# Performance work log

Hardware: AMD Instinct MI355X
Metric: run time of the kernel (lower is better)

Reference implementation:

```python
import jax, jax.numpy as jnp
import numpy as np

B, L, E, H, W = 2, 4096, 512, 8, 128
D = E // H

def _clin(x, Wr, Wi, br, bi):
    # ComplexLinear on real input: out = x@(Wr + i*Wi)^T + (br + i*bi)
    return x @ Wr.T + br, x @ Wi.T + bi

def setup_inputs() -> dict:
    key = jax.random.key(0)
    ks = jax.random.split(key, 20)
    s = 0.02
    d = {
        'query': jax.random.normal(ks[0], (B, L, E), jnp.float32),
        'key':   jax.random.normal(ks[1], (B, L, E), jnp.float32),
        'value': jax.random.normal(ks[2], (B, L, E), jnp.float32),
    }
    names = ['q', 'k', 'v', 'o']
    i = 3
    for n in names:
        d[n + 'Wr'] = jax.random.normal(ks[i], (E, E), jnp.float32) * s; i += 1
        d[n + 'Wi'] = jax.random.normal(ks[i], (E, E), jnp.float32) * s; i += 1
        d[n + 'br'] = jnp.zeros((E,), jnp.float32)
        d[n + 'bi'] = jnp.zeros((E,), jnp.float32)
    return d

def reference(query, key, value,
              qWr, qWi, qbr, qbi,
              kWr, kWi, kbr, kbi,
              vWr, vWi, vbr, vbi,
              oWr, oWi, obr, obi):
    # complex projections (real input -> complex output, kept as (re, im) float pairs)
    qr, qi = _clin(query, qWr, qWi, qbr, qbi)
    kr, ki = _clin(key,   kWr, kWi, kbr, kbi)
    vr, _vi = _clin(value, vWr, vWi, vbr, vbi)  # imag part of V is discarded by the real cast

    def heads(x):
        return x.reshape(B, L, H, D).transpose(0, 2, 1, 3)  # [B,H,L,D]
    qr, qi, kr, ki, vr = map(heads, (qr, qi, kr, ki, vr))

    # Re(q @ k^H) = qr@kr^T + qi@ki^T  (only the real part is ever used)
    scale = 1.0 / np.sqrt(D)
    scores = (jnp.einsum('bhld,bhmd->bhlm', qr, kr)
              + jnp.einsum('bhld,bhmd->bhlm', qi, ki)) * scale

    # Faithful to source: only lower_mask is applied (window_mask is built but never added).
    idx = jnp.arange(L)
    lower_mask = jnp.where(idx[:, None] - idx[None, :] >= W + 1,
                           -jnp.inf, 0.0).astype(scores.dtype)
    probs = jax.nn.softmax(scores + lower_mask, axis=-1)

    # out = probs @ v; cast to query.dtype keeps only Re = probs @ vr
    o = jnp.einsum('bhlm,bhmd->bhld', probs, vr)
    o = o.transpose(0, 2, 1, 3).reshape(B, L, E)

    out_r = o @ oWr.T + obr
    out_i = o @ oWi.T + obi
    return out_r, out_i
```

## Files before the change

kernel.cpp:

```cpp
#include <hip/hip_runtime.h>


typedef unsigned short u16;
typedef unsigned int u32;
typedef __attribute__((ext_vector_type(8))) short bf16x8;
typedef __attribute__((ext_vector_type(4))) float f32x4;
typedef __attribute__((ext_vector_type(16))) float f32x16;
typedef __attribute__((ext_vector_type(4))) u32 u32x4;

#define L_ 4096
#define E_ 512
#define M_ 8192

__device__ __forceinline__ u16 f2bf(float f) {
  union { float f; u32 u; } v; v.f = f;
  return (u16)((v.u + 0x7FFFu + ((v.u >> 16) & 1u)) >> 16);
}

__device__ __forceinline__ void gll16(const void* g, void* l) {
  __builtin_amdgcn_global_load_lds(
      (const __attribute__((address_space(1))) u32*)g,
      (__attribute__((address_space(3))) u32*)l, 16, 0, 0);
}

__global__ void cvt_x_kernel(const float* __restrict__ q, const float* __restrict__ k,
                             const float* __restrict__ v,
                             u16* __restrict__ xq, u16* __restrict__ xk, u16* __restrict__ xv) {
  const int total = 3 * (M_ * E_ / 4);
  int stride = gridDim.x * blockDim.x;
  for (int u = blockIdx.x * blockDim.x + threadIdx.x; u < total; u += stride) {
    int mat = u >> 20, e = u & ((1 << 20) - 1);
    const float4 f = ((const float4*)(mat == 0 ? q : mat == 1 ? k : v))[e];
    ushort4 o = make_ushort4(f2bf(f.x), f2bf(f.y), f2bf(f.z), f2bf(f.w));
    *(ushort4*)((mat == 0 ? xq : mat == 1 ? xk : xv) + (size_t)e * 4) = o;
  }
}

struct CPtrs { const float* w[7]; const float* b[7]; };

__global__ void cvt_wb_kernel(CPtrs p, u16* __restrict__ wcat, float* __restrict__ bcat) {
  const int total = 7 * (E_ * E_ / 4);
  int stride = gridDim.x * blockDim.x;
  int t0 = blockIdx.x * blockDim.x + threadIdx.x;
  for (int u = t0; u < total; u += stride) {
    int wi = u >> 16, e = u & 65535;
    const float4 f = ((const float4*)p.w[wi])[e];
    ushort4 o = make_ushort4(f2bf(f.x), f2bf(f.y), f2bf(f.z), f2bf(f.w));
    *(ushort4*)(wcat + (size_t)wi * 262144 + (size_t)e * 4) = o;
  }
  for (int j = t0; j < 3584; j += stride) bcat[j] = p.b[j >> 9][j & 511];
}

__device__ __forceinline__ void gemm128_main(const u16* __restrict__ A, const u16* __restrict__ Bw,
                                             int m0, int n0w, char* sm, f32x4 acc[4][4]) {
  int tid = threadIdx.x;
  int lane = tid & 63, w = tid >> 6;
  int wm = w >> 1, wn = w & 1;
#pragma unroll
  for (int a = 0; a < 4; a++)
#pragma unroll
    for (int b = 0; b < 4; b++)
#pragma unroll
      for (int j = 0; j < 4; j++) acc[a][b][j] = 0.f;

  auto stage = [&](int buf, int ks) {
    char* dst = sm + buf * 16384;
#pragma unroll
    for (int n = 0; n < 2; n++) {
      int u = n * 256 + tid;
      int row = u >> 2, c = u & 3;
      int so = (c ^ (row & 3)) * 16;
      int ldso = (n * 256 + w * 64) * 16;
      gll16((const char*)(A + (size_t)(m0 + row) * 512 + ks * 32) + so, dst + ldso);
      gll16((const char*)(Bw + (size_t)(n0w + row) * 512 + ks * 32) + so, dst + 8192 + ldso);
    }
  };

  stage(0, 0);
  __syncthreads();
  int cur = 0;
  for (int ks = 0; ks < 16; ks++) {
    if (ks < 15) stage(cur ^ 1, ks + 1);
    const char* as = sm + cur * 16384;
    const char* bs = as + 8192;
    bf16x8 af[4], bfr[4];
#pragma unroll
    for (int i = 0; i < 4; i++) {
      int ra = wm * 64 + i * 16 + (lane & 15);
      af[i] = *(const bf16x8*)(as + ra * 64 + (((lane >> 4) * 16) ^ ((ra & 3) << 4)));
      int rb = wn * 64 + i * 16 + (lane & 15);
      bfr[i] = *(const bf16x8*)(bs + rb * 64 + (((lane >> 4) * 16) ^ ((rb & 3) << 4)));
    }
    __builtin_amdgcn_s_setprio(1);
#pragma unroll
    for (int mt = 0; mt < 4; mt++)
#pragma unroll
      for (int nt = 0; nt < 4; nt++)
        acc[mt][nt] = __builtin_amdgcn_mfma_f32_16x16x32_bf16(af[mt], bfr[nt], acc[mt][nt], 0, 0, 0);
    __builtin_amdgcn_s_setprio(0);
    __syncthreads();
    cur ^= 1;
  }
}

__global__ __launch_bounds__(256) void proj_kernel(
    const u16* __restrict__ xq, const u16* __restrict__ xk, const u16* __restrict__ xv,
    const u16* __restrict__ wcat, const float* __restrict__ bcat,
    u16* __restrict__ qrb, u16* __restrict__ qib,
    u16* __restrict__ krb, u16* __restrict__ kib, u16* __restrict__ vtb) {
  __shared__ alignas(16) char sm[32768];
  int bx = blockIdx.x, by = blockIdx.y;
  const u16* A = bx < 8 ? xq : (bx < 16 ? xk : xv);
  int m0 = by * 128, n0w = bx * 128;
  f32x4 acc[4][4];
  gemm128_main(A, wcat, m0, n0w, sm, acc);

  int lane = threadIdx.x & 63, w = threadIdx.x >> 6;
  int wm = w >> 1, wn = w & 1;
  int lL = lane & 15, lH = lane >> 4;
#pragma unroll
  for (int mt = 0; mt < 4; mt++) {
#pragma unroll
    for (int nt = 0; nt < 4; nt++) {
      int n = n0w + wn * 64 + nt * 16 + lL;
      float bias = bcat[n];
      int e = n & 511;
#pragma unroll
      for (int j = 0; j < 4; j++) {
        int m = m0 + wm * 64 + mt * 16 + lH * 4 + j;
        float val = acc[mt][nt][j] + bias;
        int bb = m >> 12, ll = m & 4095;
        if (bx < 16) {
          if (bx < 8) val *= 0.18033688011112042f;
          u16* dst = (bx < 8) ? ((n & 512) ? qib : qrb) : ((n & 512) ? kib : krb);
          dst[((size_t)((bb * 8 + (e >> 6)) * 4096 + ll) << 6) + (e & 63)] = f2bf(val);
        } else {
          vtb[((size_t)((bb * 8 + (e >> 6)) * 64 + (e & 63)) << 12) + ll] = f2bf(val);
        }
      }
    }
  }
}

__global__ __launch_bounds__(256) void oproj_kernel(
    const u16* __restrict__ obf, const u16* __restrict__ wcat, const float* __restrict__ bcat,
    float* __restrict__ out) {
  __shared__ alignas(16) char sm[32768];
  int bx = blockIdx.x, by = blockIdx.y;
  int m0 = by * 128, n0w = 2560 + bx * 128;
  f32x4 acc[4][4];
  gemm128_main(obf, wcat, m0, n0w, sm, acc);

  int lane = threadIdx.x & 63, w = threadIdx.x >> 6;
  int wm = w >> 1, wn = w & 1;
  int lL = lane & 15, lH = lane >> 4;
#pragma unroll
  for (int mt = 0; mt < 4; mt++) {
#pragma unroll
    for (int nt = 0; nt < 4; nt++) {
      int n = n0w + wn * 64 + nt * 16 + lL;
      float bias = bcat[n];
      int nn = n - 2560;
      float* dst = out + ((nn & 512) ? 4194304 : 0) + (nn & 511);
#pragma unroll
      for (int j = 0; j < 4; j++) {
        int m = m0 + wm * 64 + mt * 16 + lH * 4 + j;
        dst[(size_t)m * 512] = acc[mt][nt][j] + bias;
      }
    }
  }
}

__global__ __launch_bounds__(256, 3) void attn_kernel(
    const u16* __restrict__ qrb, const u16* __restrict__ qib,
    const u16* __restrict__ krb, const u16* __restrict__ kib,
    const u16* __restrict__ vtb, u16* __restrict__ obf) {
  __shared__ alignas(16) char sm[2 * 24576];
  int bid = blockIdx.x;
  int bh = bid & 15;
  int q2 = bid >> 4;
  int qt = (q2 < 16) ? q2 : (47 - q2);
  int bb = bh >> 3, hh = bh & 7;
  int i0 = qt << 7;
  int tid = threadIdx.x;
  int lane = tid & 63, w = tid >> 6;
  int lo = lane & 31, hi = lane >> 5;
  int i0w = i0 + w * 32;
  int irow = i0w + lo;

  bf16x8 fqr[4], fqi[4];
  {
    const u16* qp = qrb + ((size_t)(bh * 4096 + irow) << 6) + hi * 8;
    const u16* qip = qib + ((size_t)(bh * 4096 + irow) << 6) + hi * 8;
#pragma unroll
    for (int c = 0; c < 4; c++) {
      fqr[c] = *(const bf16x8*)(qp + c * 16);
      fqi[c] = *(const bf16x8*)(qip + c * 16);
    }
  }

  f32x16 oa0, oa1;
#pragma unroll
  for (int r = 0; r < 16; r++) { oa0[r] = 0.f; oa1[r] = 0.f; }
  float m_run = -1e30f, l_run = 0.f;

  int jstart = (i0 >= 128) ? (i0 - 128) : 0;
  int ntiles = (4096 - jstart) >> 6;

  auto stage = [&](int buf, int j0) {
    char* dst = sm + buf * 24576;
#pragma unroll
    for (int n = 0; n < 2; n++) {
      int u = n * 256 + tid;
      int row = u >> 3, c = u & 7;
      int so = (c ^ (row & 7)) * 16;
      int ldso = (n * 256 + w * 64) * 16;
      size_t krow = ((size_t)(bh * 4096 + j0 + row) << 6);
      gll16((const char*)(krb + krow) + so, dst + ldso);
      gll16((const char*)(kib + krow) + so, dst + 8192 + ldso);
      size_t vrow = ((size_t)(bh * 64 + row) << 12) + j0;
      gll16((const char*)(vtb + vrow) + so, dst + 16384 + ldso);
    }
  };

  auto cvtpk = [](float a, float b) -> u32 {
    u32 r;
    asm("v_cvt_pk_bf16_f32 %0, %1, %2" : "=v"(r) : "v"(a), "v"(b));
    return r;
  };
  auto mkfrag = [&](const float* p, bf16x8& fA, bf16x8& fB) {
    u32 x0 = cvtpk(p[0], p[1]), y0 = cvtpk(p[4], p[5]);
    u32 x1 = cvtpk(p[2], p[3]), y1 = cvtpk(p[6], p[7]);
    u32 x2 = cvtpk(p[8], p[9]), y2 = cvtpk(p[12], p[13]);
    u32 x3 = cvtpk(p[10], p[11]), y3 = cvtpk(p[14], p[15]);
    asm("v_permlane32_swap_b32 %0, %1" : "+v"(x0), "+v"(y0));
    asm("v_permlane32_swap_b32 %0, %1" : "+v"(x1), "+v"(y1));
    asm("v_permlane32_swap_b32 %0, %1" : "+v"(x2), "+v"(y2));
    asm("v_permlane32_swap_b32 %0, %1" : "+v"(x3), "+v"(y3));
    u32x4 a; a[0] = x0; a[1] = x1; a[2] = y0; a[3] = y1;
    u32x4 b; b[0] = x2; b[1] = x3; b[2] = y2; b[3] = y3;
    fA = __builtin_bit_cast(bf16x8, a);
    fB = __builtin_bit_cast(bf16x8, b);
  };

  stage(0, jstart);
  __syncthreads();
  int cur = 0;
  int swz = (lo & 7) << 4;

  for (int t = 0; t < ntiles; t++) {
    int j0 = jstart + (t << 6);
    if (t + 1 < ntiles) stage(cur ^ 1, j0 + 64);
    const char* Kr = sm + cur * 24576;
    const char* Ki = Kr + 8192;
    const char* Vt = Kr + 16384;

    f32x16 s0, s1;
#pragma unroll
    for (int r = 0; r < 16; r++) { s0[r] = 0.f; s1[r] = 0.f; }
#pragma unroll
    for (int c = 0; c < 4; c++) {
      int off = (c * 32 + hi * 16) ^ swz;
      bf16x8 a0r = *(const bf16x8*)(Kr + lo * 128 + off);
      bf16x8 a0i = *(const bf16x8*)(Ki + lo * 128 + off);
      bf16x8 a1r = *(const bf16x8*)(Kr + (32 + lo) * 128 + off);
      bf16x8 a1i = *(const bf16x8*)(Ki + (32 + lo) * 128 + off);
      __builtin_amdgcn_s_setprio(1);
      s0 = __builtin_amdgcn_mfma_f32_32x32x16_bf16(a0r, fqr[c], s0, 0, 0, 0);
      s1 = __builtin_amdgcn_mfma_f32_32x32x16_bf16(a1r, fqr[c], s1, 0, 0, 0);
      s0 = __builtin_amdgcn_mfma_f32_32x32x16_bf16(a0i, fqi[c], s0, 0, 0, 0);
      s1 = __builtin_amdgcn_mfma_f32_32x32x16_bf16(a1i, fqi[c], s1, 0, 0, 0);
      __builtin_amdgcn_s_setprio(0);
    }
    if (j0 <= i0w - 98) {
#pragma unroll
      for (int r = 0; r < 16; r++) {
        int kk = j0 + (r & 3) + ((r >> 2) << 3) + (hi << 2);
        if (kk <= irow - 129) s0[r] = -3e38f;
        if (kk + 32 <= irow - 129) s1[r] = -3e38f;
      }
    }
    float m4[8];
#pragma unroll
    for (int j = 0; j < 4; j++)
      m4[j] = fmaxf(fmaxf(s0[4 * j], s0[4 * j + 1]), fmaxf(s0[4 * j + 2], s0[4 * j + 3]));
#pragma unroll
    for (int j = 0; j < 4; j++)
      m4[4 + j] = fmaxf(fmaxf(s1[4 * j], s1[4 * j + 1]), fmaxf(s1[4 * j + 2], s1[4 * j + 3]));
    float pmax = fmaxf(fmaxf(fmaxf(m4[0], m4[1]), fmaxf(m4[2], m4[3])),
                       fmaxf(fmaxf(m4[4], m4[5]), fmaxf(m4[6], m4[7])));
    pmax = fmaxf(pmax, __shfl_xor(pmax, 32));

    if (!__all(pmax <= m_run + 11.5f)) {
      float mnew = fmaxf(m_run, pmax);
      float scl = exp2f(m_run - mnew);
#pragma unroll
      for (int r = 0; r < 16; r++) { oa0[r] *= scl; oa1[r] *= scl; }
      l_run *= scl;
      m_run = mnew;
    }

    float ps0 = 0.f, ps1 = 0.f, ps2 = 0.f, ps3 = 0.f;
#pragma unroll
    for (int r = 0; r < 16; r += 4) {
      s0[r] = exp2f(s0[r] - m_run);     ps0 += s0[r];
      s0[r + 1] = exp2f(s0[r + 1] - m_run); ps1 += s0[r + 1];
      s0[r + 2] = exp2f(s0[r + 2] - m_run); ps2 += s0[r + 2];
      s0[r + 3] = exp2f(s0[r + 3] - m_run); ps3 += s0[r + 3];
    }
#pragma unroll
    for (int r = 0; r < 16; r += 4) {
      s1[r] = exp2f(s1[r] - m_run);     ps0 += s1[r];
      s1[r + 1] = exp2f(s1[r + 1] - m_run); ps1 += s1[r + 1];
      s1[r + 2] = exp2f(s1[r + 2] - m_run); ps2 += s1[r + 2];
      s1[r + 3] = exp2f(s1[r + 3] - m_run); ps3 += s1[r + 3];
    }
    float psum = (ps0 + ps1) + (ps2 + ps3);
    psum += __shfl_xor(psum, 32);
    l_run += psum;

    bf16x8 pf0, pf1, pf2, pf3;
    mkfrag((const float*)&s0, pf0, pf1);
    mkfrag((const float*)&s1, pf2, pf3);

#pragma unroll
    for (int kc = 0; kc < 4; kc++) {
      int off = (kc * 32 + hi * 16) ^ swz;
      bf16x8 av0 = *(const bf16x8*)(Vt + lo * 128 + off);
      bf16x8 av1 = *(const bf16x8*)(Vt + (32 + lo) * 128 + off);
      bf16x8 pk = (kc == 0) ? pf0 : (kc == 1) ? pf1 : (kc == 2) ? pf2 : pf3;
      __builtin_amdgcn_s_setprio(1);
      oa0 = __builtin_amdgcn_mfma_f32_32x32x16_bf16(av0, pk, oa0, 0, 0, 0);
      oa1 = __builtin_amdgcn_mfma_f32_32x32x16_bf16(av1, pk, oa1, 0, 0, 0);
      __builtin_amdgcn_s_setprio(0);
    }
    __syncthreads();
    cur ^= 1;
  }

  float rl = 1.0f / l_run;
  u16* orow = obf + ((size_t)(bb * 4096 + irow) << 9) + hh * 64;
#pragma unroll
  for (int g = 0; g < 4; g++) {
    ushort4 v0 = make_ushort4(f2bf(oa0[4 * g] * rl), f2bf(oa0[4 * g + 1] * rl),
                              f2bf(oa0[4 * g + 2] * rl), f2bf(oa0[4 * g + 3] * rl));
    *(ushort4*)(orow + g * 8 + hi * 4) = v0;
    ushort4 v1 = make_ushort4(f2bf(oa1[4 * g] * rl), f2bf(oa1[4 * g + 1] * rl),
                              f2bf(oa1[4 * g + 2] * rl), f2bf(oa1[4 * g + 3] * rl));
    *(ushort4*)(orow + 32 + g * 8 + hi * 4) = v1;
  }
}

extern "C" void kernel_launch(void* const* d_in, const int* in_sizes, int n_in,
                              void* d_out, int out_size, void* d_ws, size_t ws_size,
                              hipStream_t stream) {
  (void)in_sizes; (void)n_in; (void)out_size; (void)ws_size;
  const float* q = (const float*)d_in[0];
  const float* k = (const float*)d_in[1];
  const float* v = (const float*)d_in[2];
  char* ws = (char*)d_ws;
  u16* wcat = (u16*)(ws + 0x000000);
  float* bcat = (float*)(ws + 0x400000);
  u16* xq  = (u16*)(ws + 0x500000);
  u16* xk  = (u16*)(ws + 0xD00000);
  u16* xv  = (u16*)(ws + 0x1500000);
  u16* qrb = (u16*)(ws + 0x1D00000);
  u16* qib = (u16*)(ws + 0x2500000);
  u16* krb = (u16*)(ws + 0x2D00000);
  u16* kib = (u16*)(ws + 0x3500000);
  u16* vtb = (u16*)(ws + 0x3D00000);
  u16* obf = xq;
  float* out = (float*)d_out;

  cvt_x_kernel<<<2048, 256, 0, stream>>>(q, k, v, xq, xk, xv);

  CPtrs cp;
  cp.w[0] = (const float*)d_in[3];  cp.w[1] = (const float*)d_in[4];
  cp.w[2] = (const float*)d_in[7];  cp.w[3] = (const float*)d_in[8];
  cp.w[4] = (const float*)d_in[11]; cp.w[5] = (const float*)d_in[15]; cp.w[6] = (const float*)d_in[16];
  cp.b[0] = (const float*)d_in[5];  cp.b[1] = (const float*)d_in[6];
  cp.b[2] = (const float*)d_in[9];  cp.b[3] = (const float*)d_in[10];
  cp.b[4] = (const float*)d_in[13]; cp.b[5] = (const float*)d_in[17]; cp.b[6] = (const float*)d_in[18];
  cvt_wb_kernel<<<448, 256, 0, stream>>>(cp, wcat, bcat);

  proj_kernel<<<dim3(20, 64), 256, 0, stream>>>(xq, xk, xv, wcat, bcat, qrb, qib, krb, kib, vtb);
  attn_kernel<<<512, 256, 0, stream>>>(qrb, qib, krb, kib, vtb, obf);
  oproj_kernel<<<dim3(8, 64), 256, 0, stream>>>(obf, wcat, bcat, out);
}
```

Measured before the change: 201.0 us.

## Software-pipeline attention: overlap next tile's QK MFMAs with current softmax/PV

The attention loop moves from double to triple LDS buffering and is unrolled by two. Each half issues the QK^T MFMAs for the next key tile before running the masking, softmax and PV for the current tile. The aim is to hide softmax VALU/transcendental latency behind independent matrix work and keep loads two tiles ahead. The cost is more shared memory and extra live score registers, so launch bounds drop from 3 to 2 blocks per CU, which lowers occupancy.

```diff
diff --git a/kernel.cpp b/kernel.cpp
--- a/kernel.cpp
+++ b/kernel.cpp
@@ -171,11 +171,11 @@
   }
 }
 
-__global__ __launch_bounds__(256, 3) void attn_kernel(
+__global__ __launch_bounds__(256, 2) void attn_kernel(
     const u16* __restrict__ qrb, const u16* __restrict__ qib,
     const u16* __restrict__ krb, const u16* __restrict__ kib,
     const u16* __restrict__ vtb, u16* __restrict__ obf) {
-  __shared__ alignas(16) char sm[2 * 24576];
+  __shared__ alignas(16) char sm[3 * 24576];
   int bid = blockIdx.x;
   int bh = bid & 15;
   int q2 = bid >> 4;
@@ -207,8 +207,7 @@
   int jstart = (i0 >= 128) ? (i0 - 128) : 0;
   int ntiles = (4096 - jstart) >> 6;
 
-  auto stage = [&](int buf, int j0) {
-    char* dst = sm + buf * 24576;
+  auto stage = [&](char* dst, int j0) {
 #pragma unroll
     for (int n = 0; n < 2; n++) {
       int u = n * 256 + tid;
@@ -220,6 +219,29 @@
       gll16((const char*)(kib + krow) + so, dst + 8192 + ldso);
       size_t vrow = ((size_t)(bh * 64 + row) << 12) + j0;
       gll16((const char*)(vtb + vrow) + so, dst + 16384 + ldso);
+    }
+  };
+
+  int swz = (lo & 7) << 4;
+
+  auto qk = [&](const char* Kbase, f32x16& s0, f32x16& s1) {
+    const char* Kr = Kbase;
+    const char* Ki = Kbase + 8192;
+#pragma unroll
+    for (int r = 0; r < 16; r++) { s0[r] = 0.f; s1[r] = 0.f; }
+#pragma unroll
+    for (int c = 0; c < 4; c++) {
+      int off = (c * 32 + hi * 16) ^ swz;
+      bf16x8 a0r = *(const bf16x8*)(Kr + lo * 128 + off);
+      bf16x8 a0i = *(const bf16x8*)(Ki + lo * 128 + off);
+      bf16x8 a1r = *(const bf16x8*)(Kr + (32 + lo) * 128 + off);
+      bf16x8 a1i = *(const bf16x8*)(Ki + (32 + lo) * 128 + off);
+      __builtin_amdgcn_s_setprio(1);
+      s0 = __builtin_amdgcn_mfma_f32_32x32x16_bf16(a0r, fqr[c], s0, 0, 0, 0);
+      s1 = __builtin_amdgcn_mfma_f32_32x32x16_bf16(a1r, fqr[c], s1, 0, 0, 0);
+      s0 = __builtin_amdgcn_mfma_f32_32x32x16_bf16(a0i, fqi[c], s0, 0, 0, 0);
+      s1 = __builtin_amdgcn_mfma_f32_32x32x16_bf16(a1i, fqi[c], s1, 0, 0, 0);
+      __builtin_amdgcn_s_setprio(0);
     }
   };
 
@@ -243,35 +265,7 @@
     fB = __builtin_bit_cast(bf16x8, b);
   };
 
-  stage(0, jstart);
-  __syncthreads();
-  int cur = 0;
-  int swz = (lo & 7) << 4;
-
-  for (int t = 0; t < ntiles; t++) {
-    int j0 = jstart + (t << 6);
-    if (t + 1 < ntiles) stage(cur ^ 1, j0 + 64);
-    const char* Kr = sm + cur * 24576;
-    const char* Ki = Kr + 8192;
-    const char* Vt = Kr + 16384;
-
-    f32x16 s0, s1;
-#pragma unroll
-    for (int r = 0; r < 16; r++) { s0[r] = 0.f; s1[r] = 0.f; }
-#pragma unroll
-    for (int c = 0; c < 4; c++) {
-      int off = (c * 32 + hi * 16) ^ swz;
-      bf16x8 a0r = *(const bf16x8*)(Kr + lo * 128 + off);
-      bf16x8 a0i = *(const bf16x8*)(Ki + lo * 128 + off);
-      bf16x8 a1r = *(const bf16x8*)(Kr + (32 + lo) * 128 + off);
-      bf16x8 a1i = *(const bf16x8*)(Ki + (32 + lo) * 128 + off);
-      __builtin_amdgcn_s_setprio(1);
-      s0 = __builtin_amdgcn_mfma_f32_32x32x16_bf16(a0r, fqr[c], s0, 0, 0, 0);
-      s1 = __builtin_amdgcn_mfma_f32_32x32x16_bf16(a1r, fqr[c], s1, 0, 0, 0);
-      s0 = __builtin_amdgcn_mfma_f32_32x32x16_bf16(a0i, fqi[c], s0, 0, 0, 0);
-      s1 = __builtin_amdgcn_mfma_f32_32x32x16_bf16(a1i, fqi[c], s1, 0, 0, 0);
-      __builtin_amdgcn_s_setprio(0);
-    }
+  auto smpv = [&](const char* Kbase, int j0, f32x16& s0, f32x16& s1) {
     if (j0 <= i0w - 98) {
 #pragma unroll
       for (int r = 0; r < 16; r++) {
@@ -323,6 +317,7 @@
     mkfrag((const float*)&s0, pf0, pf1);
     mkfrag((const float*)&s1, pf2, pf3);
 
+    const char* Vt = Kbase + 16384;
 #pragma unroll
     for (int kc = 0; kc < 4; kc++) {
       int off = (kc * 32 + hi * 16) ^ swz;
@@ -334,8 +329,31 @@
       oa1 = __builtin_amdgcn_mfma_f32_32x32x16_bf16(av1, pk, oa1, 0, 0, 0);
       __builtin_amdgcn_s_setprio(0);
     }
+  };
+
+  char* cur = sm;
+  char* nxt = sm + 24576;
+  char* nx2 = sm + 49152;
+
+  stage(cur, jstart);
+  stage(nxt, jstart + 64);
+  __syncthreads();
+
+  f32x16 sA0, sA1, sB0, sB1;
+  qk(cur, sA0, sA1);
+
+  for (int t = 0; t < ntiles; t += 2) {
+    int j0 = jstart + (t << 6);
+    if (t + 2 < ntiles) stage(nx2, j0 + 128);
+    qk(nxt, sB0, sB1);
+    smpv(cur, j0, sA0, sA1);
     __syncthreads();
-    cur ^= 1;
+    { char* tmp = cur; cur = nxt; nxt = nx2; nx2 = tmp; }
+    if (t + 3 < ntiles) stage(nx2, j0 + 192);
+    if (t + 2 < ntiles) qk(nxt, sA0, sA1);
+    smpv(cur, j0 + 64, sB0, sB1);
+    __syncthreads();
+    { char* tmp = cur; cur = nxt; nxt = nx2; nx2 = tmp; }
   }
 
   float rl = 1.0f / l_run;
```

New measurement: 197.5 us. No clear change (-1.7%).
